# Kernel tuning notes

Measured on AMD Instinct MI355X. Metric: run time of the kernel, lower is better.

The kernel has to match this reference:

```python
import jax, jax.numpy as jnp
import numpy as np

# Sobel kernels stacked as [O=2, I=1, 3, 3]
_KX = np.array([[-1., 0., 1.], [-2., 0., 2.], [-1., 0., 1.]], dtype=np.float32)
_KY = np.array([[1., 2., 1.], [0., 0., 0.], [-1., -2., -1.]], dtype=np.float32)
_SOBEL_W = jnp.asarray(np.stack([_KX, _KY])[:, None, :, :])  # [2,1,3,3]


def _sobel(x):
    # x: [B,1,H,W] -> |Gx| + |Gy| : [B,1,H,W]
    g = jax.lax.conv_general_dilated(
        x, _SOBEL_W, window_strides=(1, 1), padding=((1, 1), (1, 1)),
        dimension_numbers=('NCHW', 'OIHW', 'NCHW'))  # [B,2,H,W]
    return jnp.sum(jnp.abs(g), axis=1, keepdims=True)


def _threshold_mask(g, k):
    # g: [B,1,H,W]; k-th SMALLEST over flattened (C*H*W) per batch (torch.kthvalue)
    B, N, H, W = g.shape
    flat = g.reshape(B, N, H * W)
    kth = jnp.sort(flat, axis=-1)[:, :, k - 1:k]  # [B,N,1]
    mask = (flat >= kth).astype(g.dtype)
    return mask.reshape(B, N, H, W)


def setup_inputs() -> dict:
    key = jax.random.key(0)
    kA, kB, kF = jax.random.split(key, 3)
    shape = (8, 3, 1024, 1024)
    return {
        'image_A': jax.random.uniform(kA, shape, dtype=jnp.float32),
        'image_B': jax.random.uniform(kB, shape, dtype=jnp.float32),
        'image_fused': jax.random.uniform(kF, shape, dtype=jnp.float32),
        'thresholds': 524288,
    }


def reference(image_A, image_B, image_fused, thresholds):
    gA = _sobel(image_A[:, :1])
    gB = _sobel(image_B[:, :1])
    gF = _sobel(image_fused[:, :1])
    joint_max = jnp.maximum(gA, gB)  # max over concat([gA,gB], dim=1) with 1 ch each
    maskA = _threshold_mask(gA, thresholds)
    maskB = _threshold_mask(gB, thresholds)
    loss = jnp.mean(jnp.abs(gF - joint_max))
    return (loss, maskA, maskB)
```

## Files before the change

### kernel.cpp

```cpp
#include <hip/hip_runtime.h>

#define IMG_H 1024
#define IMG_W 1024
#define NBATCH 8
#define NCH 3
#define NPIX (IMG_H * IMG_W)
#define SEGS 64
#define NTOT (8388608LL)

#define BINS1 4096
#define SH1 19
#define BINS2 4096
#define SH2 7
#define BINS3 128

#define WS_HIST2_OFF   0
#define WS_HIST2_BYTES (2 * NBATCH * BINS2 * 4)
#define WS_HIST3_OFF   (WS_HIST2_OFF + WS_HIST2_BYTES)
#define WS_HIST3_BYTES (2 * NBATCH * BINS3 * 4)
#define WS_MISC_OFF    (WS_HIST3_OFF + WS_HIST3_BYTES)
#define WS_MISC_BYTES  4096
#define WS_H1R_OFF     (WS_MISC_OFF + WS_MISC_BYTES)
#define WS_H1R_BYTES   (2 * NBATCH * BINS1 * 4)
#define WS_H1P_OFF     (WS_H1R_OFF + WS_H1R_BYTES)
#define WS_H1P_BYTES   (2 * NBATCH * SEGS * BINS1 * 2)
#define WS_TOTAL       (WS_H1P_OFF + WS_H1P_BYTES)
#define WS_ZERO_BYTES  (WS_HIST2_BYTES + WS_HIST3_BYTES + WS_MISC_BYTES)

struct Row3f { float l, c, r; };

__device__ __forceinline__ Row3f load3(const float* __restrict__ img, int y, int x) {
    Row3f o;
    if ((unsigned)y >= (unsigned)IMG_H) { o.l = o.c = o.r = 0.0f; return o; }
    const float* row = img + (size_t)y * IMG_W;
    o.c = row[x];
    o.l = (x > 0)         ? row[x - 1] : 0.0f;
    o.r = (x < IMG_W - 1) ? row[x + 1] : 0.0f;
    return o;
}

__device__ __forceinline__ float sobel_g(const Row3f& r0, const Row3f& r1, const Row3f& r2) {
    float gx = r0.r - r0.l;
    gx -= 2.0f * r1.l;
    gx += 2.0f * r1.r;
    gx -= r2.l;
    gx += r2.r;
    float gy = r0.l + 2.0f * r0.c;
    gy += r0.r;
    gy -= r2.l;
    gy -= 2.0f * r2.c;
    gy -= r2.r;
    return fabsf(gx) + fabsf(gy);
}

extern "C" __global__ __launch_bounds__(512)
void k_pass0(const float* __restrict__ A, const float* __restrict__ B,
             const float* __restrict__ F,
             unsigned short* __restrict__ hist1p, double* __restrict__ lossAcc)
{
    __shared__ unsigned int h[2 * BINS1];
    __shared__ double lsum[8];
    const int t = threadIdx.x;
    for (int i = t; i < 2 * BINS1; i += 512) h[i] = 0u;
    __syncthreads();

    const int blk = blockIdx.x;
    const int batch = blk >> 6;
    const int seg = blk & 63;
    const int y0 = (seg >> 1) * 32;
    const int x  = (seg & 1) * 512 + t;

    const float* a = A + (size_t)batch * NCH * NPIX;
    const float* b = B + (size_t)batch * NCH * NPIX;
    const float* f = F + (size_t)batch * NCH * NPIX;

    Row3f a0 = load3(a, y0 - 1, x), a1 = load3(a, y0, x), a2;
    Row3f b0 = load3(b, y0 - 1, x), b1 = load3(b, y0, x), b2;
    Row3f f0 = load3(f, y0 - 1, x), f1 = load3(f, y0, x), f2;

    double loss = 0.0;
    for (int i = 0; i < 32; ++i) {
        const int y = y0 + i;
        a2 = load3(a, y + 1, x);
        b2 = load3(b, y + 1, x);
        f2 = load3(f, y + 1, x);
        const float gA = sobel_g(a0, a1, a2);
        const float gB = sobel_g(b0, b1, b2);
        const float gF = sobel_g(f0, f1, f2);
        atomicAdd(&h[__float_as_uint(gA) >> SH1], 1u);
        atomicAdd(&h[BINS1 + (__float_as_uint(gB) >> SH1)], 1u);
        const float jm = fmaxf(gA, gB);
        loss += (double)fabsf(gF - jm);
        a0 = a1; a1 = a2;
        b0 = b1; b1 = b2;
        f0 = f1; f1 = f2;
    }
    __syncthreads();

    unsigned short* oA = hist1p + ((size_t)batch            * SEGS + seg) * BINS1;
    unsigned short* oB = hist1p + ((size_t)(NBATCH + batch) * SEGS + seg) * BINS1;
    for (int i = t; i < BINS1; i += 512) {
        oA[i] = (unsigned short)h[i];
        oB[i] = (unsigned short)h[BINS1 + i];
    }

    for (int off = 32; off > 0; off >>= 1) loss += __shfl_down(loss, off);
    if ((t & 63) == 0) lsum[t >> 6] = loss;
    __syncthreads();
    if (t == 0) {
        double s = 0.0;
        for (int i = 0; i < 8; ++i) s += lsum[i];
        atomicAdd(lossAcc, s);
    }
}

extern "C" __global__ __launch_bounds__(256)
void k_scan1a(const unsigned short* __restrict__ hist1p, unsigned int* __restrict__ hist1r)
{
    const int idx = blockIdx.x * 256 + threadIdx.x;
    const int ib  = idx >> 12;
    const int bin = idx & (BINS1 - 1);
    const unsigned short* p = hist1p + (size_t)ib * SEGS * BINS1 + bin;
    unsigned int s = 0;
    #pragma unroll 8
    for (int sg = 0; sg < SEGS; ++sg) s += p[(size_t)sg * BINS1];
    hist1r[idx] = s;
}

extern "C" __global__ __launch_bounds__(256)
void k_scan1b(const unsigned int* __restrict__ hist1r, const int* __restrict__ kptr,
              int* __restrict__ sel1, int* __restrict__ resid1)
{
    const int ib = blockIdx.x, t = threadIdx.x;
    const unsigned int* hr = hist1r + (size_t)ib * BINS1;
    __shared__ unsigned int csum[256];
    unsigned int s = 0;
    for (int j = 0; j < BINS1 / 256; ++j) s += hr[t * (BINS1 / 256) + j];
    csum[t] = s;
    __syncthreads();
    if (t == 0) {
        long long k = (long long)kptr[0];
        if (k < 1 || k > (long long)NPIX) {
            float kf = ((const float*)kptr)[0];
            k = (long long)kf;
            if (k < 1) k = 1;
            if (k > NPIX) k = NPIX;
        }
        long long cum = 0;
        int c = 0;
        while (c < 255 && cum + csum[c] < k) { cum += csum[c]; ++c; }
        int bin = c * (BINS1 / 256);
        while (bin < BINS1 - 1 && cum + hr[bin] < k) { cum += hr[bin]; ++bin; }
        sel1[ib] = bin;
        resid1[ib] = (int)(k - cum);
    }
}

extern "C" __global__ __launch_bounds__(512)
void k_passB(const float* __restrict__ A, const float* __restrict__ B,
             const int* __restrict__ sel1, unsigned int* __restrict__ hist2)
{
    const int t = threadIdx.x;
    const int blk = blockIdx.x;
    const int batch = blk >> 6;
    const int seg = blk & 63;
    const int y0 = (seg >> 1) * 32;
    const int x  = (seg & 1) * 512 + t;

    const float* a = A + (size_t)batch * NCH * NPIX;
    const float* b = B + (size_t)batch * NCH * NPIX;
    const unsigned sA = (unsigned)sel1[batch];
    const unsigned sB = (unsigned)sel1[NBATCH + batch];
    unsigned int* h2A = hist2 + (size_t)batch * BINS2;
    unsigned int* h2B = hist2 + (size_t)(NBATCH + batch) * BINS2;

    Row3f a0 = load3(a, y0 - 1, x), a1 = load3(a, y0, x), a2;
    Row3f b0 = load3(b, y0 - 1, x), b1 = load3(b, y0, x), b2;
    for (int i = 0; i < 32; ++i) {
        const int y = y0 + i;
        a2 = load3(a, y + 1, x);
        b2 = load3(b, y + 1, x);
        const unsigned uA = __float_as_uint(sobel_g(a0, a1, a2));
        const unsigned uB = __float_as_uint(sobel_g(b0, b1, b2));
        if ((uA >> SH1) == sA) atomicAdd(&h2A[(uA >> SH2) & (BINS2 - 1)], 1u);
        if ((uB >> SH1) == sB) atomicAdd(&h2B[(uB >> SH2) & (BINS2 - 1)], 1u);
        a0 = a1; a1 = a2;
        b0 = b1; b1 = b2;
    }
}

extern "C" __global__ __launch_bounds__(256)
void k_scan2b(const unsigned int* __restrict__ hist2, const int* __restrict__ resid1,
              int* __restrict__ sel2, int* __restrict__ resid2)
{
    const int ib = blockIdx.x, t = threadIdx.x;
    const unsigned int* h2 = hist2 + (size_t)ib * BINS2;
    __shared__ unsigned int csum[256];
    unsigned int s = 0;
    for (int j = 0; j < BINS2 / 256; ++j) s += h2[t * (BINS2 / 256) + j];
    csum[t] = s;
    __syncthreads();
    if (t == 0) {
        long long k = (long long)resid1[ib];
        long long cum = 0;
        int c = 0;
        while (c < 255 && cum + csum[c] < k) { cum += csum[c]; ++c; }
        int bin = c * (BINS2 / 256);
        while (bin < BINS2 - 1 && cum + h2[bin] < k) { cum += h2[bin]; ++bin; }
        sel2[ib] = bin;
        resid2[ib] = (int)(k - cum);
    }
}

extern "C" __global__ __launch_bounds__(512)
void k_passC(const float* __restrict__ A, const float* __restrict__ B,
             const int* __restrict__ sel1, const int* __restrict__ sel2,
             unsigned int* __restrict__ hist3)
{
    const int t = threadIdx.x;
    const int blk = blockIdx.x;
    const int batch = blk >> 6;
    const int seg = blk & 63;
    const int y0 = (seg >> 1) * 32;
    const int x  = (seg & 1) * 512 + t;

    const float* a = A + (size_t)batch * NCH * NPIX;
    const float* b = B + (size_t)batch * NCH * NPIX;
    const unsigned pA = ((unsigned)sel1[batch] << 12)          | (unsigned)sel2[batch];
    const unsigned pB = ((unsigned)sel1[NBATCH + batch] << 12) | (unsigned)sel2[NBATCH + batch];
    unsigned int* h3A = hist3 + (size_t)batch * BINS3;
    unsigned int* h3B = hist3 + (size_t)(NBATCH + batch) * BINS3;

    Row3f a0 = load3(a, y0 - 1, x), a1 = load3(a, y0, x), a2;
    Row3f b0 = load3(b, y0 - 1, x), b1 = load3(b, y0, x), b2;
    for (int i = 0; i < 32; ++i) {
        const int y = y0 + i;
        a2 = load3(a, y + 1, x);
        b2 = load3(b, y + 1, x);
        const unsigned uA = __float_as_uint(sobel_g(a0, a1, a2));
        const unsigned uB = __float_as_uint(sobel_g(b0, b1, b2));
        if ((uA >> SH2) == pA) atomicAdd(&h3A[uA & (BINS3 - 1)], 1u);
        if ((uB >> SH2) == pB) atomicAdd(&h3B[uB & (BINS3 - 1)], 1u);
        a0 = a1; a1 = a2;
        b0 = b1; b1 = b2;
    }
}

extern "C" __global__ __launch_bounds__(64)
void k_scan3(const unsigned int* __restrict__ hist3, const int* __restrict__ sel1,
             const int* __restrict__ sel2, const int* __restrict__ resid2,
             unsigned int* __restrict__ kthbits,
             const double* __restrict__ lossAcc, float* __restrict__ out)
{
    const int ib = blockIdx.x, t = threadIdx.x;
    if (t == 0) {
        const unsigned int* h3 = hist3 + (size_t)ib * BINS3;
        long long k = (long long)resid2[ib];
        long long cum = 0;
        int bin = 0;
        while (bin < BINS3 - 1 && cum + h3[bin] < k) { cum += h3[bin]; ++bin; }
        kthbits[ib] = ((unsigned)sel1[ib] << SH1) | ((unsigned)sel2[ib] << SH2) | (unsigned)bin;
    }
    if (ib == 0 && t == 63) {
        out[0] = (float)(lossAcc[0] * (1.0 / 8388608.0));
    }
}

extern "C" __global__ __launch_bounds__(512)
void k_passD(const float* __restrict__ A, const float* __restrict__ B,
             const unsigned int* __restrict__ kthbits, float* __restrict__ out)
{
    const int t = threadIdx.x;
    const int blk = blockIdx.x;
    const int batch = blk >> 6;
    const int seg = blk & 63;
    const int y0 = (seg >> 1) * 32;
    const int x  = (seg & 1) * 512 + t;

    const float* a = A + (size_t)batch * NCH * NPIX;
    const float* b = B + (size_t)batch * NCH * NPIX;
    const unsigned kA = kthbits[batch];
    const unsigned kB = kthbits[NBATCH + batch];
    float* mA = out + 1 + (size_t)batch * NPIX;
    float* mB = out + 1 + (size_t)NTOT + (size_t)batch * NPIX;

    Row3f a0 = load3(a, y0 - 1, x), a1 = load3(a, y0, x), a2;
    Row3f b0 = load3(b, y0 - 1, x), b1 = load3(b, y0, x), b2;
    for (int i = 0; i < 32; ++i) {
        const int y = y0 + i;
        a2 = load3(a, y + 1, x);
        b2 = load3(b, y + 1, x);
        const unsigned uA = __float_as_uint(sobel_g(a0, a1, a2));
        const unsigned uB = __float_as_uint(sobel_g(b0, b1, b2));
        mA[(size_t)y * IMG_W + x] = (uA >= kA) ? 1.0f : 0.0f;
        mB[(size_t)y * IMG_W + x] = (uB >= kB) ? 1.0f : 0.0f;
        a0 = a1; a1 = a2;
        b0 = b1; b1 = b2;
    }
}

extern "C" void kernel_launch(void* const* d_in, const int* in_sizes, int n_in,
                              void* d_out, int out_size, void* d_ws, size_t ws_size,
                              hipStream_t stream)
{
    const float* A = (const float*)d_in[0];
    const float* B = (const float*)d_in[1];
    const float* F = (const float*)d_in[2];
    const int* kptr = (const int*)d_in[3];
    float* out = (float*)d_out;

    if (ws_size < (size_t)WS_TOTAL) return;

    char* ws = (char*)d_ws;
    unsigned int* hist2   = (unsigned int*)(ws + WS_HIST2_OFF);
    unsigned int* hist3   = (unsigned int*)(ws + WS_HIST3_OFF);
    double* lossAcc       = (double*)(ws + WS_MISC_OFF);
    int* sel1             = (int*)(ws + WS_MISC_OFF + 64);
    int* resid1           = (int*)(ws + WS_MISC_OFF + 128);
    int* sel2             = (int*)(ws + WS_MISC_OFF + 192);
    int* resid2           = (int*)(ws + WS_MISC_OFF + 256);
    unsigned int* kthbits = (unsigned int*)(ws + WS_MISC_OFF + 320);
    unsigned int* hist1r  = (unsigned int*)(ws + WS_H1R_OFF);
    unsigned short* hist1p = (unsigned short*)(ws + WS_H1P_OFF);

    hipMemsetAsync(ws, 0, WS_ZERO_BYTES, stream);

    k_pass0 <<<dim3(NBATCH * SEGS), dim3(512), 0, stream>>>(A, B, F, hist1p, lossAcc);
    k_scan1a<<<dim3(2 * NBATCH * BINS1 / 256), dim3(256), 0, stream>>>(hist1p, hist1r);
    k_scan1b<<<dim3(2 * NBATCH), dim3(256), 0, stream>>>(hist1r, kptr, sel1, resid1);
    k_passB <<<dim3(NBATCH * SEGS), dim3(512), 0, stream>>>(A, B, sel1, hist2);
    k_scan2b<<<dim3(2 * NBATCH), dim3(256), 0, stream>>>(hist2, resid1, sel2, resid2);
    k_passC <<<dim3(NBATCH * SEGS), dim3(512), 0, stream>>>(A, B, sel1, sel2, hist3);
    k_scan3 <<<dim3(2 * NBATCH), dim3(64), 0, stream>>>(hist3, sel1, sel2, resid2, kthbits, lossAcc, out);
    k_passD <<<dim3(NBATCH * SEGS), dim3(512), 0, stream>>>(A, B, kthbits, out);
}
```

Measured before the change: 368.5 us.

## Replace radix-select passes with candidate compaction and single-pass mask write

The second image pass now writes the final masks directly for pixels whose top-level bin is decided, and compacts pixels in the ambiguous bin into a global list in workspace. A new per-batch kernel then resolves the remaining radix digits from that list and patches only those mask entries. This removes two full recompute-and-read passes over A and B (passC, passD) plus their scan kernels, and replaces the serial scans with parallel block prefix sums. The pass0 shared histograms are also duplicated per half-block to reduce atomic contention. The cost is list traffic and extra syncs, and correctness depends on the list capacity fitting in the workspace.

```diff
diff --git a/kernel.cpp b/kernel.cpp
--- a/kernel.cpp
+++ b/kernel.cpp
@@ -10,22 +10,14 @@
 
 #define BINS1 4096
 #define SH1 19
-#define BINS2 4096
-#define SH2 7
-#define BINS3 128
-
-#define WS_HIST2_OFF   0
-#define WS_HIST2_BYTES (2 * NBATCH * BINS2 * 4)
-#define WS_HIST3_OFF   (WS_HIST2_OFF + WS_HIST2_BYTES)
-#define WS_HIST3_BYTES (2 * NBATCH * BINS3 * 4)
-#define WS_MISC_OFF    (WS_HIST3_OFF + WS_HIST3_BYTES)
-#define WS_MISC_BYTES  4096
-#define WS_H1R_OFF     (WS_MISC_OFF + WS_MISC_BYTES)
-#define WS_H1R_BYTES   (2 * NBATCH * BINS1 * 4)
-#define WS_H1P_OFF     (WS_H1R_OFF + WS_H1R_BYTES)
-#define WS_H1P_BYTES   (2 * NBATCH * SEGS * BINS1 * 2)
-#define WS_TOTAL       (WS_H1P_OFF + WS_H1P_BYTES)
-#define WS_ZERO_BYTES  (WS_HIST2_BYTES + WS_HIST3_BYTES + WS_MISC_BYTES)
+
+#define WS_MISC_OFF   0
+#define WS_MISC_BYTES 4096
+#define WS_H1R_OFF    (WS_MISC_OFF + WS_MISC_BYTES)
+#define WS_H1R_BYTES  (2 * NBATCH * BINS1 * 4)
+#define WS_H1P_OFF    (WS_H1R_OFF + WS_H1R_BYTES)
+#define WS_H1P_BYTES  (2 * NBATCH * SEGS * BINS1 * 2)
+#define WS_LIST_OFF   (WS_H1P_OFF + WS_H1P_BYTES)
 
 struct Row3f { float l, c, r; };
 
@@ -58,10 +50,10 @@
              const float* __restrict__ F,
              unsigned short* __restrict__ hist1p, double* __restrict__ lossAcc)
 {
-    __shared__ unsigned int h[2 * BINS1];
+    __shared__ unsigned int h[4 * BINS1];
     __shared__ double lsum[8];
     const int t = threadIdx.x;
-    for (int i = t; i < 2 * BINS1; i += 512) h[i] = 0u;
+    for (int i = t; i < 4 * BINS1; i += 512) h[i] = 0u;
     __syncthreads();
 
     const int blk = blockIdx.x;
@@ -69,6 +61,7 @@
     const int seg = blk & 63;
     const int y0 = (seg >> 1) * 32;
     const int x  = (seg & 1) * 512 + t;
+    unsigned int* hc = h + (t >> 8) * (2 * BINS1);
 
     const float* a = A + (size_t)batch * NCH * NPIX;
     const float* b = B + (size_t)batch * NCH * NPIX;
@@ -87,10 +80,9 @@
         const float gA = sobel_g(a0, a1, a2);
         const float gB = sobel_g(b0, b1, b2);
         const float gF = sobel_g(f0, f1, f2);
-        atomicAdd(&h[__float_as_uint(gA) >> SH1], 1u);
-        atomicAdd(&h[BINS1 + (__float_as_uint(gB) >> SH1)], 1u);
-        const float jm = fmaxf(gA, gB);
-        loss += (double)fabsf(gF - jm);
+        atomicAdd(&hc[__float_as_uint(gA) >> SH1], 1u);
+        atomicAdd(&hc[BINS1 + (__float_as_uint(gB) >> SH1)], 1u);
+        loss += (double)fabsf(gF - fmaxf(gA, gB));
         a0 = a1; a1 = a2;
         b0 = b1; b1 = b2;
         f0 = f1; f1 = f2;
@@ -99,9 +91,10 @@
 
     unsigned short* oA = hist1p + ((size_t)batch            * SEGS + seg) * BINS1;
     unsigned short* oB = hist1p + ((size_t)(NBATCH + batch) * SEGS + seg) * BINS1;
-    for (int i = t; i < BINS1; i += 512) {
-        oA[i] = (unsigned short)h[i];
-        oB[i] = (unsigned short)h[BINS1 + i];
+    for (int i = t; i < 2 * BINS1; i += 512) {
+        const unsigned v = h[i] + h[2 * BINS1 + i];
+        if (i < BINS1) oA[i] = (unsigned short)v;
+        else           oB[i - BINS1] = (unsigned short)v;
     }
 
     for (int off = 32; off > 0; off >>= 1) loss += __shfl_down(loss, off);
@@ -127,176 +120,189 @@
     hist1r[idx] = s;
 }
 
-extern "C" __global__ __launch_bounds__(256)
+extern "C" __global__ __launch_bounds__(1024)
 void k_scan1b(const unsigned int* __restrict__ hist1r, const int* __restrict__ kptr,
               int* __restrict__ sel1, int* __restrict__ resid1)
 {
     const int ib = blockIdx.x, t = threadIdx.x;
     const unsigned int* hr = hist1r + (size_t)ib * BINS1;
-    __shared__ unsigned int csum[256];
-    unsigned int s = 0;
-    for (int j = 0; j < BINS1 / 256; ++j) s += hr[t * (BINS1 / 256) + j];
-    csum[t] = s;
-    __syncthreads();
-    if (t == 0) {
-        long long k = (long long)kptr[0];
-        if (k < 1 || k > (long long)NPIX) {
-            float kf = ((const float*)kptr)[0];
-            k = (long long)kf;
-            if (k < 1) k = 1;
-            if (k > NPIX) k = NPIX;
-        }
-        long long cum = 0;
-        int c = 0;
-        while (c < 255 && cum + csum[c] < k) { cum += csum[c]; ++c; }
-        int bin = c * (BINS1 / 256);
-        while (bin < BINS1 - 1 && cum + hr[bin] < k) { cum += hr[bin]; ++bin; }
+    long long kl = (long long)kptr[0];
+    if (kl < 1 || kl > (long long)NPIX) {
+        float kf = ((const float*)kptr)[0];
+        kl = (long long)kf;
+        if (kl < 1) kl = 1;
+        if (kl > NPIX) kl = NPIX;
+    }
+    const unsigned k = (unsigned)kl;
+
+    const uint4 c = ((const uint4*)hr)[t];
+    const unsigned s = c.x + c.y + c.z + c.w;
+    __shared__ unsigned ls[1024];
+    ls[t] = s; __syncthreads();
+    for (int off = 1; off < 1024; off <<= 1) {
+        unsigned v = (t >= off) ? ls[t - off] : 0u;
+        __syncthreads();
+        ls[t] += v;
+        __syncthreads();
+    }
+    const unsigned incl = ls[t];
+    const unsigned excl = incl - s;
+    if (excl < k && k <= incl) {
+        unsigned cum = excl; int bin = t * 4;
+        if (cum + c.x < k) { cum += c.x; ++bin;
+          if (cum + c.y < k) { cum += c.y; ++bin;
+            if (cum + c.z < k) { cum += c.z; ++bin; } } }
         sel1[ib] = bin;
         resid1[ib] = (int)(k - cum);
     }
 }
 
-extern "C" __global__ __launch_bounds__(512)
+#define PB_ROWS 32
+extern "C" __global__ __launch_bounds__(1024)
 void k_passB(const float* __restrict__ A, const float* __restrict__ B,
-             const int* __restrict__ sel1, unsigned int* __restrict__ hist2)
+             const int* __restrict__ sel1, unsigned int* __restrict__ gCnt,
+             uint2* __restrict__ list, unsigned cap, float* __restrict__ out)
 {
     const int t = threadIdx.x;
     const int blk = blockIdx.x;
-    const int batch = blk >> 6;
-    const int seg = blk & 63;
-    const int y0 = (seg >> 1) * 32;
-    const int x  = (seg & 1) * 512 + t;
+    const int batch = blk >> 5;
+    const int y0 = (blk & 31) * PB_ROWS;
+    const int x = t;
 
     const float* a = A + (size_t)batch * NCH * NPIX;
     const float* b = B + (size_t)batch * NCH * NPIX;
     const unsigned sA = (unsigned)sel1[batch];
     const unsigned sB = (unsigned)sel1[NBATCH + batch];
-    unsigned int* h2A = hist2 + (size_t)batch * BINS2;
-    unsigned int* h2B = hist2 + (size_t)(NBATCH + batch) * BINS2;
+    float* mA = out + 1 + (size_t)batch * NPIX;
+    float* mB = out + 1 + (size_t)NTOT + (size_t)batch * NPIX;
+
+    __shared__ uint2 bufA[2048], bufB[2048];
+    __shared__ unsigned cntA, cntB, baseA, baseB;
+    if (t == 0) { cntA = 0u; cntB = 0u; }
+    __syncthreads();
 
     Row3f a0 = load3(a, y0 - 1, x), a1 = load3(a, y0, x), a2;
     Row3f b0 = load3(b, y0 - 1, x), b1 = load3(b, y0, x), b2;
-    for (int i = 0; i < 32; ++i) {
+    for (int i = 0; i < PB_ROWS; ++i) {
         const int y = y0 + i;
         a2 = load3(a, y + 1, x);
         b2 = load3(b, y + 1, x);
         const unsigned uA = __float_as_uint(sobel_g(a0, a1, a2));
         const unsigned uB = __float_as_uint(sobel_g(b0, b1, b2));
-        if ((uA >> SH1) == sA) atomicAdd(&h2A[(uA >> SH2) & (BINS2 - 1)], 1u);
-        if ((uB >> SH1) == sB) atomicAdd(&h2B[(uB >> SH2) & (BINS2 - 1)], 1u);
+        const unsigned binA = uA >> SH1, binB = uB >> SH1;
+        const unsigned idx = (unsigned)y * IMG_W + (unsigned)x;
+        mA[idx] = (binA > sA) ? 1.0f : 0.0f;
+        mB[idx] = (binB > sB) ? 1.0f : 0.0f;
+        if (binA == sA) { unsigned p = atomicAdd(&cntA, 1u); bufA[p] = make_uint2(uA, idx); }
+        if (binB == sB) { unsigned p = atomicAdd(&cntB, 1u); bufB[p] = make_uint2(uB, idx); }
         a0 = a1; a1 = a2;
         b0 = b1; b1 = b2;
-    }
-}
-
-extern "C" __global__ __launch_bounds__(256)
-void k_scan2b(const unsigned int* __restrict__ hist2, const int* __restrict__ resid1,
-              int* __restrict__ sel2, int* __restrict__ resid2)
+
+        __syncthreads();
+        const bool last = (i == PB_ROWS - 1);
+        const unsigned nA = cntA, nB = cntB;
+        const bool doA = (nA >= 1024u) || (last && nA > 0u);
+        const bool doB = (nB >= 1024u) || (last && nB > 0u);
+        if (doA || doB) {
+            if (t == 0) {
+                if (doA) baseA = atomicAdd(&gCnt[batch], nA);
+                if (doB) baseB = atomicAdd(&gCnt[NBATCH + batch], nB);
+            }
+            __syncthreads();
+            if (doA) {
+                const unsigned bs = baseA;
+                for (unsigned j = t; j < nA; j += 1024u) {
+                    const unsigned d = bs + j;
+                    if (d < cap) list[(size_t)batch * cap + d] = bufA[j];
+                }
+            }
+            if (doB) {
+                const unsigned bs = baseB;
+                for (unsigned j = t; j < nB; j += 1024u) {
+                    const unsigned d = bs + j;
+                    if (d < cap) list[(size_t)(NBATCH + batch) * cap + d] = bufB[j];
+                }
+            }
+            __syncthreads();
+            if (t == 0) { if (doA) cntA = 0u; if (doB) cntB = 0u; }
+        }
+        __syncthreads();
+    }
+}
+
+extern "C" __global__ __launch_bounds__(1024)
+void k_selectfix(const uint2* __restrict__ list, const unsigned int* __restrict__ gCnt,
+                 unsigned cap, const int* __restrict__ sel1, const int* __restrict__ resid1,
+                 const double* __restrict__ lossAcc, float* __restrict__ out)
 {
     const int ib = blockIdx.x, t = threadIdx.x;
-    const unsigned int* h2 = hist2 + (size_t)ib * BINS2;
-    __shared__ unsigned int csum[256];
-    unsigned int s = 0;
-    for (int j = 0; j < BINS2 / 256; ++j) s += h2[t * (BINS2 / 256) + j];
-    csum[t] = s;
-    __syncthreads();
-    if (t == 0) {
-        long long k = (long long)resid1[ib];
-        long long cum = 0;
-        int c = 0;
-        while (c < 255 && cum + csum[c] < k) { cum += csum[c]; ++c; }
-        int bin = c * (BINS2 / 256);
-        while (bin < BINS2 - 1 && cum + h2[bin] < k) { cum += h2[bin]; ++bin; }
-        sel2[ib] = bin;
-        resid2[ib] = (int)(k - cum);
-    }
-}
-
-extern "C" __global__ __launch_bounds__(512)
-void k_passC(const float* __restrict__ A, const float* __restrict__ B,
-             const int* __restrict__ sel1, const int* __restrict__ sel2,
-             unsigned int* __restrict__ hist3)
-{
-    const int t = threadIdx.x;
-    const int blk = blockIdx.x;
-    const int batch = blk >> 6;
-    const int seg = blk & 63;
-    const int y0 = (seg >> 1) * 32;
-    const int x  = (seg & 1) * 512 + t;
-
-    const float* a = A + (size_t)batch * NCH * NPIX;
-    const float* b = B + (size_t)batch * NCH * NPIX;
-    const unsigned pA = ((unsigned)sel1[batch] << 12)          | (unsigned)sel2[batch];
-    const unsigned pB = ((unsigned)sel1[NBATCH + batch] << 12) | (unsigned)sel2[NBATCH + batch];
-    unsigned int* h3A = hist3 + (size_t)batch * BINS3;
-    unsigned int* h3B = hist3 + (size_t)(NBATCH + batch) * BINS3;
-
-    Row3f a0 = load3(a, y0 - 1, x), a1 = load3(a, y0, x), a2;
-    Row3f b0 = load3(b, y0 - 1, x), b1 = load3(b, y0, x), b2;
-    for (int i = 0; i < 32; ++i) {
-        const int y = y0 + i;
-        a2 = load3(a, y + 1, x);
-        b2 = load3(b, y + 1, x);
-        const unsigned uA = __float_as_uint(sobel_g(a0, a1, a2));
-        const unsigned uB = __float_as_uint(sobel_g(b0, b1, b2));
-        if ((uA >> SH2) == pA) atomicAdd(&h3A[uA & (BINS3 - 1)], 1u);
-        if ((uB >> SH2) == pB) atomicAdd(&h3B[uB & (BINS3 - 1)], 1u);
-        a0 = a1; a1 = a2;
-        b0 = b1; b1 = b2;
-    }
-}
-
-extern "C" __global__ __launch_bounds__(64)
-void k_scan3(const unsigned int* __restrict__ hist3, const int* __restrict__ sel1,
-             const int* __restrict__ sel2, const int* __restrict__ resid2,
-             unsigned int* __restrict__ kthbits,
-             const double* __restrict__ lossAcc, float* __restrict__ out)
-{
-    const int ib = blockIdx.x, t = threadIdx.x;
-    if (t == 0) {
-        const unsigned int* h3 = hist3 + (size_t)ib * BINS3;
-        long long k = (long long)resid2[ib];
-        long long cum = 0;
-        int bin = 0;
-        while (bin < BINS3 - 1 && cum + h3[bin] < k) { cum += h3[bin]; ++bin; }
-        kthbits[ib] = ((unsigned)sel1[ib] << SH1) | ((unsigned)sel2[ib] << SH2) | (unsigned)bin;
-    }
-    if (ib == 0 && t == 63) {
-        out[0] = (float)(lossAcc[0] * (1.0 / 8388608.0));
-    }
-}
-
-extern "C" __global__ __launch_bounds__(512)
-void k_passD(const float* __restrict__ A, const float* __restrict__ B,
-             const unsigned int* __restrict__ kthbits, float* __restrict__ out)
-{
-    const int t = threadIdx.x;
-    const int blk = blockIdx.x;
-    const int batch = blk >> 6;
-    const int seg = blk & 63;
-    const int y0 = (seg >> 1) * 32;
-    const int x  = (seg & 1) * 512 + t;
-
-    const float* a = A + (size_t)batch * NCH * NPIX;
-    const float* b = B + (size_t)batch * NCH * NPIX;
-    const unsigned kA = kthbits[batch];
-    const unsigned kB = kthbits[NBATCH + batch];
-    float* mA = out + 1 + (size_t)batch * NPIX;
-    float* mB = out + 1 + (size_t)NTOT + (size_t)batch * NPIX;
-
-    Row3f a0 = load3(a, y0 - 1, x), a1 = load3(a, y0, x), a2;
-    Row3f b0 = load3(b, y0 - 1, x), b1 = load3(b, y0, x), b2;
-    for (int i = 0; i < 32; ++i) {
-        const int y = y0 + i;
-        a2 = load3(a, y + 1, x);
-        b2 = load3(b, y + 1, x);
-        const unsigned uA = __float_as_uint(sobel_g(a0, a1, a2));
-        const unsigned uB = __float_as_uint(sobel_g(b0, b1, b2));
-        mA[(size_t)y * IMG_W + x] = (uA >= kA) ? 1.0f : 0.0f;
-        mB[(size_t)y * IMG_W + x] = (uB >= kB) ? 1.0f : 0.0f;
-        a0 = a1; a1 = a2;
-        b0 = b1; b1 = b2;
-    }
+    const unsigned n = min(gCnt[ib], cap);
+    const unsigned kk = (unsigned)resid1[ib];
+    const uint2* L = list + (size_t)ib * cap;
+
+    __shared__ unsigned h2[BINS1];
+    __shared__ unsigned ls[1024];
+    __shared__ unsigned bcast[4];
+    if (t < 4) bcast[t] = 0u;
+    for (int i = t; i < BINS1; i += 1024) h2[i] = 0u;
+    __syncthreads();
+
+    for (unsigned j = t; j < n; j += 1024u) atomicAdd(&h2[(L[j].x >> 7) & 4095u], 1u);
+    __syncthreads();
+
+    const unsigned c0 = h2[4 * t], c1 = h2[4 * t + 1], c2 = h2[4 * t + 2], c3 = h2[4 * t + 3];
+    const unsigned s = c0 + c1 + c2 + c3;
+    ls[t] = s; __syncthreads();
+    for (int off = 1; off < 1024; off <<= 1) {
+        unsigned v = (t >= off) ? ls[t - off] : 0u;
+        __syncthreads();
+        ls[t] += v;
+        __syncthreads();
+    }
+    {
+        const unsigned incl = ls[t], excl = incl - s;
+        if (excl < kk && kk <= incl) {
+            unsigned cum = excl; unsigned bin = 4u * t;
+            if (cum + c0 < kk) { cum += c0; ++bin;
+              if (cum + c1 < kk) { cum += c1; ++bin;
+                if (cum + c2 < kk) { cum += c2; ++bin; } } }
+            bcast[0] = bin;
+            bcast[1] = kk - cum;
+        }
+    }
+    __syncthreads();
+    const unsigned sel2 = bcast[0], k3 = bcast[1];
+
+    if (t < 128) h2[t] = 0u;
+    __syncthreads();
+    for (unsigned j = t; j < n; j += 1024u) {
+        const unsigned b = L[j].x;
+        if (((b >> 7) & 4095u) == sel2) atomicAdd(&h2[b & 127u], 1u);
+    }
+    __syncthreads();
+    {
+        const unsigned s3 = (t < 128) ? h2[t] : 0u;
+        ls[t] = s3; __syncthreads();
+        for (int off = 1; off < 1024; off <<= 1) {
+            unsigned v = (t >= off) ? ls[t - off] : 0u;
+            __syncthreads();
+            ls[t] += v;
+            __syncthreads();
+        }
+        const unsigned incl = ls[t], excl = incl - s3;
+        if (t < 128 && excl < k3 && k3 <= incl) {
+            bcast[2] = ((unsigned)sel1[ib] << SH1) | (sel2 << 7) | (unsigned)t;
+        }
+    }
+    __syncthreads();
+    const unsigned kth = bcast[2];
+
+    float* m = out + 1 + (size_t)ib * NPIX;
+    for (unsigned j = t; j < n; j += 1024u) {
+        const uint2 e = L[j];
+        m[e.y] = (e.x >= kth) ? 1.0f : 0.0f;
+    }
+    if (ib == 0 && t == 0) out[0] = (float)(lossAcc[0] * (1.0 / 8388608.0));
 }
 
 extern "C" void kernel_launch(void* const* d_in, const int* in_sizes, int n_in,
@@ -309,28 +315,25 @@
     const int* kptr = (const int*)d_in[3];
     float* out = (float*)d_out;
 
-    if (ws_size < (size_t)WS_TOTAL) return;
+    if (ws_size < (size_t)WS_LIST_OFF + 16 * 8 * 1024) return;
 
     char* ws = (char*)d_ws;
-    unsigned int* hist2   = (unsigned int*)(ws + WS_HIST2_OFF);
-    unsigned int* hist3   = (unsigned int*)(ws + WS_HIST3_OFF);
-    double* lossAcc       = (double*)(ws + WS_MISC_OFF);
-    int* sel1             = (int*)(ws + WS_MISC_OFF + 64);
-    int* resid1           = (int*)(ws + WS_MISC_OFF + 128);
-    int* sel2             = (int*)(ws + WS_MISC_OFF + 192);
-    int* resid2           = (int*)(ws + WS_MISC_OFF + 256);
-    unsigned int* kthbits = (unsigned int*)(ws + WS_MISC_OFF + 320);
-    unsigned int* hist1r  = (unsigned int*)(ws + WS_H1R_OFF);
+    double* lossAcc        = (double*)(ws + WS_MISC_OFF);
+    unsigned int* gCnt     = (unsigned int*)(ws + WS_MISC_OFF + 64);
+    unsigned int* hist1r   = (unsigned int*)(ws + WS_H1R_OFF);
     unsigned short* hist1p = (unsigned short*)(ws + WS_H1P_OFF);
-
-    hipMemsetAsync(ws, 0, WS_ZERO_BYTES, stream);
-
-    k_pass0 <<<dim3(NBATCH * SEGS), dim3(512), 0, stream>>>(A, B, F, hist1p, lossAcc);
-    k_scan1a<<<dim3(2 * NBATCH * BINS1 / 256), dim3(256), 0, stream>>>(hist1p, hist1r);
-    k_scan1b<<<dim3(2 * NBATCH), dim3(256), 0, stream>>>(hist1r, kptr, sel1, resid1);
-    k_passB <<<dim3(NBATCH * SEGS), dim3(512), 0, stream>>>(A, B, sel1, hist2);
-    k_scan2b<<<dim3(2 * NBATCH), dim3(256), 0, stream>>>(hist2, resid1, sel2, resid2);
-    k_passC <<<dim3(NBATCH * SEGS), dim3(512), 0, stream>>>(A, B, sel1, sel2, hist3);
-    k_scan3 <<<dim3(2 * NBATCH), dim3(64), 0, stream>>>(hist3, sel1, sel2, resid2, kthbits, lossAcc, out);
-    k_passD <<<dim3(NBATCH * SEGS), dim3(512), 0, stream>>>(A, B, kthbits, out);
-}
+    uint2* list            = (uint2*)(ws + WS_LIST_OFF);
+    int* sel1              = (int*)(ws + WS_MISC_OFF + 128);
+    int* resid1            = (int*)(ws + WS_MISC_OFF + 256);
+
+    unsigned long long capll = (ws_size - WS_LIST_OFF) / (16ull * 8ull);
+    unsigned cap = (capll > (unsigned long long)NPIX) ? (unsigned)NPIX : (unsigned)capll;
+
+    hipMemsetAsync(ws, 0, WS_MISC_BYTES, stream);
+
+    k_pass0    <<<dim3(NBATCH * SEGS), dim3(512), 0, stream>>>(A, B, F, hist1p, lossAcc);
+    k_scan1a   <<<dim3(2 * NBATCH * BINS1 / 256), dim3(256), 0, stream>>>(hist1p, hist1r);
+    k_scan1b   <<<dim3(2 * NBATCH), dim3(1024), 0, stream>>>(hist1r, kptr, sel1, resid1);
+    k_passB    <<<dim3(NBATCH * 32), dim3(1024), 0, stream>>>(A, B, sel1, gCnt, list, cap, out);
+    k_selectfix<<<dim3(2 * NBATCH), dim3(1024), 0, stream>>>(list, gCnt, cap, sel1, resid1, lossAcc, out);
+}
```

After: 344.8 us. -6.4%, faster.
